# Kernel optimization log

Measured on AMD Instinct MI355X. Metric: run time of the kernel, lower is better.

Reference implementation:

```python
import jax, jax.numpy as jnp
import numpy as np

OBS, ACT, LAT, H = 64, 32, 25, 5
B = 8192
SUP_H = 64


def setup_inputs() -> dict:
    key = jax.random.key(0)
    ks = jax.random.split(key, 12)
    s = 0.1
    inp = {
        'obs': jax.random.normal(ks[0], (B, OBS), jnp.float32),
        # supervisor FeedForward: OBS -> 64 -> 64 -> LAT, ReLU hidden, Sigmoid output
        'sw1': jax.random.normal(ks[1], (OBS, SUP_H), jnp.float32) * s,
        'sb1': jnp.zeros((SUP_H,), jnp.float32),
        'sw2': jax.random.normal(ks[2], (SUP_H, SUP_H), jnp.float32) * s,
        'sb2': jnp.zeros((SUP_H,), jnp.float32),
        'sw3': jax.random.normal(ks[3], (SUP_H, LAT), jnp.float32) * s,
        'sb3': jnp.zeros((LAT,), jnp.float32),
        # OBS*ACT tiny reflex FeedForwards 1 -> H -> 1, stacked into batched params
        'rw1': jax.random.normal(ks[4], (OBS, ACT, H), jnp.float32) * s,
        'rb1': jnp.zeros((OBS, ACT, H), jnp.float32),
        'rw2': jax.random.normal(ks[5], (OBS, ACT, H), jnp.float32) * s,
        'rb2': jnp.zeros((OBS, ACT), jnp.float32),
        # activation matrix (LAT, OBS, ACT)
        'act_matrix': jnp.ones((LAT, OBS, ACT), jnp.float32),
    }
    return inp


def reference(obs, sw1, sb1, sw2, sb2, sw3, sb3, rw1, rb1, rw2, rb2, act_matrix):
    # supervisor: (B, LAT) sigmoid latent activations
    h = jax.nn.relu(obs @ sw1 + sb1)
    h = jax.nn.relu(h @ sw2 + sb2)
    latent = jax.nn.sigmoid(h @ sw3 + sb3)

    # reflex gating: (B, LAT) x (LAT, OBS, ACT) -> (B, OBS, ACT), softmax over ACT
    logits = jnp.einsum('bl,loa->boa', latent, act_matrix)
    reflex_acts = jax.nn.softmax(logits, axis=-1)

    # all OBS*ACT tiny 1->H->1 MLPs, batched: input is obs[:, o] (scalar per net)
    # hidden: (B, OBS, ACT, H)
    rh = jax.nn.relu(obs[:, :, None, None] * rw1[None] + rb1[None])
    reflex_out = jnp.einsum('boah,oah->boa', rh, rw2) + rb2[None]  # (B, OBS, ACT)

    # weighted sum over obs dim -> (B, ACT)
    return jnp.sum(reflex_out * reflex_acts, axis=1)
```

## Files before the change

### kernel.cpp

```cpp
#include <hip/hip_runtime.h>


#define TOBS 64
#define TACT 32
#define TLAT 25
#define TH   5
#define TB   8192
#define BT   16
#define OCH  8
#define NCHUNK (TOBS / OCH)
#define LATP 29
#define OSTR 68

__device__ __forceinline__ float sigmoidf_(float x) {
    return 1.0f / (1.0f + __expf(-x));
}

__global__ __launch_bounds__(256, 2)
void reflex_fused(const float* __restrict__ obs,
                  const float* __restrict__ sw1, const float* __restrict__ sb1,
                  const float* __restrict__ sw2, const float* __restrict__ sb2,
                  const float* __restrict__ sw3, const float* __restrict__ sb3,
                  const float* __restrict__ rw1, const float* __restrict__ rb1,
                  const float* __restrict__ rw2, const float* __restrict__ rb2,
                  const float* __restrict__ am,  float* __restrict__ out)
{
    __shared__ __align__(16) float obs_s[BT * OSTR];
    __shared__ __align__(16) float h1_s[BT * OSTR];
    __shared__ __align__(16) float h2_s[BT * OSTR];
    __shared__ __align__(16) float lat_s[BT * 28];
    __shared__ __align__(16) float sb1_s[64];
    __shared__ __align__(16) float sb2_s[64];
    __shared__ __align__(16) float sb3_s[32];
    __shared__ __align__(16) union {
        struct { float w1[64 * 64]; float w2[64 * 64]; float w3[64 * 26]; } p1;
        struct { float At[OCH * TACT * LATP];
                 float w1[TH * OCH * TACT]; float b1[TH * OCH * TACT];
                 float w2[TH * OCH * TACT]; float b2[OCH * TACT]; } p2;
    } U;

    const int tid  = threadIdx.x;
    const int row0 = blockIdx.x * BT;

    for (int i = tid; i < BT * TOBS; i += 256) {
        int r = i >> 6, k = i & 63;
        obs_s[r * OSTR + k] = obs[(row0 + r) * TOBS + k];
    }
    for (int i = tid; i < 64 * 64; i += 256) U.p1.w1[i] = sw1[i];
    for (int i = tid; i < 64 * 64; i += 256) U.p1.w2[i] = sw2[i];
    for (int i = tid; i < 64 * 25; i += 256) {
        int k = i / 25, j = i - k * 25;
        U.p1.w3[k * 26 + j] = sw3[i];
    }
    if (tid < 64) { sb1_s[tid] = sb1[tid]; sb2_s[tid] = sb2[tid]; }
    if (tid < 32) sb3_s[tid] = (tid < TLAT) ? sb3[tid] : 0.0f;
    __syncthreads();

    {
        const int r = tid >> 4, q = tid & 15, j0 = q * 4;
        float a0 = sb1_s[j0], a1 = sb1_s[j0 + 1], a2 = sb1_s[j0 + 2], a3 = sb1_s[j0 + 3];
        #pragma unroll 8
        for (int k = 0; k < 64; ++k) {
            float x = obs_s[r * OSTR + k];
            const float4 w = *(const float4*)&U.p1.w1[k * 64 + j0];
            a0 = fmaf(x, w.x, a0); a1 = fmaf(x, w.y, a1);
            a2 = fmaf(x, w.z, a2); a3 = fmaf(x, w.w, a3);
        }
        float4 hv = make_float4(fmaxf(a0, 0.f), fmaxf(a1, 0.f), fmaxf(a2, 0.f), fmaxf(a3, 0.f));
        *(float4*)&h1_s[r * OSTR + j0] = hv;
    }
    __syncthreads();

    {
        const int r = tid >> 4, q = tid & 15, j0 = q * 4;
        float a0 = sb2_s[j0], a1 = sb2_s[j0 + 1], a2 = sb2_s[j0 + 2], a3 = sb2_s[j0 + 3];
        #pragma unroll 8
        for (int k = 0; k < 64; ++k) {
            float x = h1_s[r * OSTR + k];
            const float4 w = *(const float4*)&U.p1.w2[k * 64 + j0];
            a0 = fmaf(x, w.x, a0); a1 = fmaf(x, w.y, a1);
            a2 = fmaf(x, w.z, a2); a3 = fmaf(x, w.w, a3);
        }
        float4 hv = make_float4(fmaxf(a0, 0.f), fmaxf(a1, 0.f), fmaxf(a2, 0.f), fmaxf(a3, 0.f));
        *(float4*)&h2_s[r * OSTR + j0] = hv;
    }
    __syncthreads();

    {
        const int r = tid >> 4, q = tid & 15, j = q * 2;
        float a0 = sb3_s[j & 31], a1 = sb3_s[(j + 1) & 31];
        #pragma unroll 8
        for (int k = 0; k < 64; ++k) {
            float x = h2_s[r * OSTR + k];
            a0 = fmaf(x, U.p1.w3[k * 26 + j], a0);
            a1 = fmaf(x, U.p1.w3[k * 26 + j + 1], a1);
        }
        if (j < TLAT)     lat_s[r * 28 + j]     = sigmoidf_(a0);
        if (j + 1 < TLAT) lat_s[r * 28 + j + 1] = sigmoidf_(a1);
    }
    __syncthreads();

    const int lane = tid & 63;
    const int a    = lane & 31;
    const int hw   = tid >> 5;
    const int r0   = hw * 2, r1 = hw * 2 + 1;

    float latA[TLAT], latB[TLAT];
    #pragma unroll
    for (int l = 0; l < TLAT; ++l) {
        latA[l] = lat_s[r0 * 28 + l];
        latB[l] = lat_s[r1 * 28 + l];
    }
    float acc0 = 0.f, acc1 = 0.f;

    for (int c = 0; c < NCHUNK; ++c) {
        const int o0 = c * OCH;
        __syncthreads();

        {
            const int oc = tid >> 5, a_ = tid & 31;
            const int o  = o0 + oc;
            #pragma unroll
            for (int l = 0; l < TLAT; ++l)
                U.p2.At[tid * LATP + l] = am[(l * TOBS + o) * TACT + a_];
        }
        for (int i = tid; i < TH * OCH * TACT; i += 256) {
            int h = i >> 8, j = i & 255;
            int o = o0 + (j >> 5), a_ = j & 31;
            int gi = (o * TACT + a_) * TH + h;
            U.p2.w1[i] = rw1[gi];
            U.p2.b1[i] = rb1[gi];
            U.p2.w2[i] = rw2[gi];
        }
        for (int i = tid; i < OCH * TACT; i += 256)
            U.p2.b2[i] = rb2[(o0 + (i >> 5)) * TACT + (i & 31)];
        __syncthreads();

        for (int oc = 0; oc < OCH; ++oc) {
            const int o  = o0 + oc;
            const int jb = oc * TACT + a;

            float l0 = 0.f, l1 = 0.f;
            const int ab = jb * LATP;
            #pragma unroll
            for (int l = 0; l < TLAT; ++l) {
                float Av = U.p2.At[ab + l];
                l0 = fmaf(Av, latA[l], l0);
                l1 = fmaf(Av, latB[l], l1);
            }
            float e0 = __expf(l0), e1 = __expf(l1);

            float s0 = e0, s1 = e1;
            #pragma unroll
            for (int d = 16; d >= 1; d >>= 1) {
                s0 += __shfl_xor(s0, d);
                s1 += __shfl_xor(s1, d);
            }
            float p0 = e0 * __builtin_amdgcn_rcpf(s0);
            float p1 = e1 * __builtin_amdgcn_rcpf(s1);

            float x0 = obs_s[r0 * OSTR + o], x1 = obs_s[r1 * OSTR + o];
            float ro0 = U.p2.b2[jb], ro1 = ro0;
            #pragma unroll
            for (int h = 0; h < TH; ++h) {
                float w1v = U.p2.w1[h * 256 + jb];
                float b1v = U.p2.b1[h * 256 + jb];
                float w2v = U.p2.w2[h * 256 + jb];
                float t0 = fmaxf(fmaf(x0, w1v, b1v), 0.f);
                float t1 = fmaxf(fmaf(x1, w1v, b1v), 0.f);
                ro0 = fmaf(t0, w2v, ro0);
                ro1 = fmaf(t1, w2v, ro1);
            }
            acc0 = fmaf(ro0, p0, acc0);
            acc1 = fmaf(ro1, p1, acc1);
        }
    }

    out[(row0 + r0) * TACT + a] = acc0;
    out[(row0 + r1) * TACT + a] = acc1;
}

extern "C" void kernel_launch(void* const* d_in, const int* in_sizes, int n_in,
                              void* d_out, int out_size, void* d_ws, size_t ws_size,
                              hipStream_t stream) {
    const float* obs = (const float*)d_in[0];
    const float* sw1 = (const float*)d_in[1];
    const float* sb1 = (const float*)d_in[2];
    const float* sw2 = (const float*)d_in[3];
    const float* sb2 = (const float*)d_in[4];
    const float* sw3 = (const float*)d_in[5];
    const float* sb3 = (const float*)d_in[6];
    const float* rw1 = (const float*)d_in[7];
    const float* rb1 = (const float*)d_in[8];
    const float* rw2 = (const float*)d_in[9];
    const float* rb2 = (const float*)d_in[10];
    const float* am  = (const float*)d_in[11];
    float* out = (float*)d_out;

    reflex_fused<<<TB / BT, 256, 0, stream>>>(obs, sw1, sb1, sw2, sb2, sw3, sb3,
                                              rw1, rb1, rw2, rb2, am, out);
}
```

Measured before the change: 63.64 us.

## Double-buffer reflex parameter chunks with register prefetch and DPP reductions

The reflex-stage chunks (activation matrix slice and per-net weights) are now double-buffered: the next chunk is loaded from global memory into registers while the current chunk is computed, then written to the alternate shared buffer, which halves the barriers per chunk. Supervisor MLP weights are read straight from global memory instead of being staged in shared memory, which shrinks shared usage. Shared layouts are padded so each thread reads its data with float4 loads, and the softmax sum uses DPP/swizzle instead of shuffles. The risks are higher register pressure from the prefetch arrays and more global weight traffic in the MLP stages.

```diff
diff --git a/kernel.cpp b/kernel.cpp
--- a/kernel.cpp
+++ b/kernel.cpp
@@ -7,10 +7,24 @@
 #define TH   5
 #define TB   8192
 #define BT   16
-#define OCH  8
-#define NCHUNK (TOBS / OCH)
-#define LATP 29
-#define OSTR 68
+#define OCH  4
+#define NCH  16
+#define ATS  28
+#define WTS  20
+#define HSTR 68
+
+#define DPP_ADD(x, ctrl) \
+  ((x) + __builtin_bit_cast(float, __builtin_amdgcn_update_dpp( \
+      0, __builtin_bit_cast(int, (x)), (ctrl), 0xF, 0xF, true)))
+
+__device__ __forceinline__ float halfwave_sum(float x) {
+    x = DPP_ADD(x, 0xB1);
+    x = DPP_ADD(x, 0x4E);
+    x = DPP_ADD(x, 0x141);
+    x = DPP_ADD(x, 0x140);
+    int y = __builtin_amdgcn_ds_swizzle(__builtin_bit_cast(int, x), 0x401F);
+    return x + __builtin_bit_cast(float, y);
+}
 
 __device__ __forceinline__ float sigmoidf_(float x) {
     return 1.0f / (1.0f + __expf(-x));
@@ -25,154 +39,187 @@
                   const float* __restrict__ rw2, const float* __restrict__ rb2,
                   const float* __restrict__ am,  float* __restrict__ out)
 {
-    __shared__ __align__(16) float obs_s[BT * OSTR];
-    __shared__ __align__(16) float h1_s[BT * OSTR];
-    __shared__ __align__(16) float h2_s[BT * OSTR];
-    __shared__ __align__(16) float lat_s[BT * 28];
-    __shared__ __align__(16) float sb1_s[64];
-    __shared__ __align__(16) float sb2_s[64];
-    __shared__ __align__(16) float sb3_s[32];
+    __shared__ __align__(16) float obs_s[BT * HSTR];
+    __shared__ __align__(16) float lat_s[BT * 26];
     __shared__ __align__(16) union {
-        struct { float w1[64 * 64]; float w2[64 * 64]; float w3[64 * 26]; } p1;
-        struct { float At[OCH * TACT * LATP];
-                 float w1[TH * OCH * TACT]; float b1[TH * OCH * TACT];
-                 float w2[TH * OCH * TACT]; float b2[OCH * TACT]; } p2;
+        struct { float h1[BT * HSTR]; float h2[BT * HSTR]; } p1;
+        struct { float At[2][128 * ATS]; float Wt[2][128 * WTS]; } p2;
     } U;
 
     const int tid  = threadIdx.x;
     const int row0 = blockIdx.x * BT;
 
-    for (int i = tid; i < BT * TOBS; i += 256) {
-        int r = i >> 6, k = i & 63;
-        obs_s[r * OSTR + k] = obs[(row0 + r) * TOBS + k];
-    }
-    for (int i = tid; i < 64 * 64; i += 256) U.p1.w1[i] = sw1[i];
-    for (int i = tid; i < 64 * 64; i += 256) U.p1.w2[i] = sw2[i];
-    for (int i = tid; i < 64 * 25; i += 256) {
-        int k = i / 25, j = i - k * 25;
-        U.p1.w3[k * 26 + j] = sw3[i];
-    }
-    if (tid < 64) { sb1_s[tid] = sb1[tid]; sb2_s[tid] = sb2[tid]; }
-    if (tid < 32) sb3_s[tid] = (tid < TLAT) ? sb3[tid] : 0.0f;
-    __syncthreads();
-
-    {
-        const int r = tid >> 4, q = tid & 15, j0 = q * 4;
-        float a0 = sb1_s[j0], a1 = sb1_s[j0 + 1], a2 = sb1_s[j0 + 2], a3 = sb1_s[j0 + 3];
+    {
+        const int r = tid >> 4, f = tid & 15;
+        *(float4*)&obs_s[r * HSTR + f * 4] =
+            *(const float4*)&obs[(row0 + r) * TOBS + f * 4];
+    }
+    __syncthreads();
+
+    {
+        const int r = tid >> 4, j0 = (tid & 15) * 4;
+        float4 acc = *(const float4*)&sb1[j0];
         #pragma unroll 8
         for (int k = 0; k < 64; ++k) {
-            float x = obs_s[r * OSTR + k];
-            const float4 w = *(const float4*)&U.p1.w1[k * 64 + j0];
-            a0 = fmaf(x, w.x, a0); a1 = fmaf(x, w.y, a1);
-            a2 = fmaf(x, w.z, a2); a3 = fmaf(x, w.w, a3);
-        }
-        float4 hv = make_float4(fmaxf(a0, 0.f), fmaxf(a1, 0.f), fmaxf(a2, 0.f), fmaxf(a3, 0.f));
-        *(float4*)&h1_s[r * OSTR + j0] = hv;
-    }
-    __syncthreads();
-
-    {
-        const int r = tid >> 4, q = tid & 15, j0 = q * 4;
-        float a0 = sb2_s[j0], a1 = sb2_s[j0 + 1], a2 = sb2_s[j0 + 2], a3 = sb2_s[j0 + 3];
+            float x = obs_s[r * HSTR + k];
+            const float4 w = *(const float4*)&sw1[k * 64 + j0];
+            acc.x = fmaf(x, w.x, acc.x); acc.y = fmaf(x, w.y, acc.y);
+            acc.z = fmaf(x, w.z, acc.z); acc.w = fmaf(x, w.w, acc.w);
+        }
+        *(float4*)&U.p1.h1[r * HSTR + j0] =
+            make_float4(fmaxf(acc.x, 0.f), fmaxf(acc.y, 0.f),
+                        fmaxf(acc.z, 0.f), fmaxf(acc.w, 0.f));
+    }
+    __syncthreads();
+
+    {
+        const int r = tid >> 4, j0 = (tid & 15) * 4;
+        float4 acc = *(const float4*)&sb2[j0];
         #pragma unroll 8
         for (int k = 0; k < 64; ++k) {
-            float x = h1_s[r * OSTR + k];
-            const float4 w = *(const float4*)&U.p1.w2[k * 64 + j0];
-            a0 = fmaf(x, w.x, a0); a1 = fmaf(x, w.y, a1);
-            a2 = fmaf(x, w.z, a2); a3 = fmaf(x, w.w, a3);
-        }
-        float4 hv = make_float4(fmaxf(a0, 0.f), fmaxf(a1, 0.f), fmaxf(a2, 0.f), fmaxf(a3, 0.f));
-        *(float4*)&h2_s[r * OSTR + j0] = hv;
-    }
-    __syncthreads();
-
-    {
-        const int r = tid >> 4, q = tid & 15, j = q * 2;
-        float a0 = sb3_s[j & 31], a1 = sb3_s[(j + 1) & 31];
-        #pragma unroll 8
-        for (int k = 0; k < 64; ++k) {
-            float x = h2_s[r * OSTR + k];
-            a0 = fmaf(x, U.p1.w3[k * 26 + j], a0);
-            a1 = fmaf(x, U.p1.w3[k * 26 + j + 1], a1);
-        }
-        if (j < TLAT)     lat_s[r * 28 + j]     = sigmoidf_(a0);
-        if (j + 1 < TLAT) lat_s[r * 28 + j + 1] = sigmoidf_(a1);
-    }
-    __syncthreads();
-
-    const int lane = tid & 63;
-    const int a    = lane & 31;
-    const int hw   = tid >> 5;
-    const int r0   = hw * 2, r1 = hw * 2 + 1;
-
+            float x = U.p1.h1[r * HSTR + k];
+            const float4 w = *(const float4*)&sw2[k * 64 + j0];
+            acc.x = fmaf(x, w.x, acc.x); acc.y = fmaf(x, w.y, acc.y);
+            acc.z = fmaf(x, w.z, acc.z); acc.w = fmaf(x, w.w, acc.w);
+        }
+        *(float4*)&U.p1.h2[r * HSTR + j0] =
+            make_float4(fmaxf(acc.x, 0.f), fmaxf(acc.y, 0.f),
+                        fmaxf(acc.z, 0.f), fmaxf(acc.w, 0.f));
+    }
+    __syncthreads();
+
+    {
+        const int r = tid >> 4, q = tid & 15;
+        if (q < 13) {
+            const int j = q * 2;
+            float a0 = sb3[j];
+            float a1 = (j + 1 < TLAT) ? sb3[j + 1] : 0.f;
+            #pragma unroll 8
+            for (int k = 0; k < 64; ++k) {
+                float x = U.p1.h2[r * HSTR + k];
+                a0 = fmaf(x, sw3[k * TLAT + j], a0);
+                if (j + 1 < TLAT) a1 = fmaf(x, sw3[k * TLAT + j + 1], a1);
+            }
+            lat_s[r * 26 + j] = sigmoidf_(a0);
+            if (j + 1 < TLAT) lat_s[r * 26 + j + 1] = sigmoidf_(a1);
+        }
+    }
+
+    const int a  = tid & 31;
+    const int hw = tid >> 5;
+    const int r0 = hw * 2, r1 = r0 + 1;
+
+    float pA[13], pW[8], pB2 = 0.f;
+
+    auto stage_load = [&](int c) {
+        const int o0 = c * OCH;
+        const float* amc = am + o0 * TACT;
+        #pragma unroll
+        for (int t = 0; t < 13; ++t) {
+            int i = tid + t * 256;
+            if (i < 3200) {
+                int l = i >> 7, jb = i & 127;
+                pA[t] = amc[l * (TOBS * TACT) + jb];
+            }
+        }
+        const int base160 = o0 * 160;
+        #pragma unroll
+        for (int t = 0; t < 8; ++t) {
+            int i = tid + t * 256;
+            if (i < 1920) {
+                int arr = i / 640, rem = i - arr * 640;
+                const float* p = (arr == 0) ? rw1 : ((arr == 1) ? rb1 : rw2);
+                pW[t] = p[base160 + rem];
+            }
+        }
+        if (tid < 128) pB2 = rb2[o0 * TACT + tid];
+    };
+
+    auto stage_write = [&](int b) {
+        float* Ab = U.p2.At[b];
+        #pragma unroll
+        for (int t = 0; t < 13; ++t) {
+            int i = tid + t * 256;
+            if (i < 3200) {
+                int l = i >> 7, jb = i & 127;
+                Ab[jb * ATS + l] = pA[t];
+            }
+        }
+        float* Wb = U.p2.Wt[b];
+        #pragma unroll
+        for (int t = 0; t < 8; ++t) {
+            int i = tid + t * 256;
+            if (i < 1920) {
+                int arr = i / 640, rem = i - arr * 640;
+                int g = rem / 5, h = rem - g * 5;
+                Wb[g * WTS + arr * 5 + h] = pW[t];
+            }
+        }
+        if (tid < 128) Wb[tid * WTS + 15] = pB2;
+    };
+
+    stage_load(0);
+    __syncthreads();
     float latA[TLAT], latB[TLAT];
     #pragma unroll
     for (int l = 0; l < TLAT; ++l) {
-        latA[l] = lat_s[r0 * 28 + l];
-        latB[l] = lat_s[r1 * 28 + l];
-    }
+        latA[l] = lat_s[r0 * 26 + l];
+        latB[l] = lat_s[r1 * 26 + l];
+    }
+    stage_write(0);
+    __syncthreads();
+
     float acc0 = 0.f, acc1 = 0.f;
 
-    for (int c = 0; c < NCHUNK; ++c) {
-        const int o0 = c * OCH;
-        __syncthreads();
+    for (int c = 0; c < NCH; ++c) {
+        if (c + 1 < NCH) stage_load(c + 1);
 
         {
-            const int oc = tid >> 5, a_ = tid & 31;
-            const int o  = o0 + oc;
+            const float* Ab = U.p2.At[c & 1];
+            const float* Wb = U.p2.Wt[c & 1];
             #pragma unroll
-            for (int l = 0; l < TLAT; ++l)
-                U.p2.At[tid * LATP + l] = am[(l * TOBS + o) * TACT + a_];
-        }
-        for (int i = tid; i < TH * OCH * TACT; i += 256) {
-            int h = i >> 8, j = i & 255;
-            int o = o0 + (j >> 5), a_ = j & 31;
-            int gi = (o * TACT + a_) * TH + h;
-            U.p2.w1[i] = rw1[gi];
-            U.p2.b1[i] = rb1[gi];
-            U.p2.w2[i] = rw2[gi];
-        }
-        for (int i = tid; i < OCH * TACT; i += 256)
-            U.p2.b2[i] = rb2[(o0 + (i >> 5)) * TACT + (i & 31)];
-        __syncthreads();
-
-        for (int oc = 0; oc < OCH; ++oc) {
-            const int o  = o0 + oc;
-            const int jb = oc * TACT + a;
-
-            float l0 = 0.f, l1 = 0.f;
-            const int ab = jb * LATP;
-            #pragma unroll
-            for (int l = 0; l < TLAT; ++l) {
-                float Av = U.p2.At[ab + l];
-                l0 = fmaf(Av, latA[l], l0);
-                l1 = fmaf(Av, latB[l], l1);
-            }
-            float e0 = __expf(l0), e1 = __expf(l1);
-
-            float s0 = e0, s1 = e1;
-            #pragma unroll
-            for (int d = 16; d >= 1; d >>= 1) {
-                s0 += __shfl_xor(s0, d);
-                s1 += __shfl_xor(s1, d);
-            }
-            float p0 = e0 * __builtin_amdgcn_rcpf(s0);
-            float p1 = e1 * __builtin_amdgcn_rcpf(s1);
-
-            float x0 = obs_s[r0 * OSTR + o], x1 = obs_s[r1 * OSTR + o];
-            float ro0 = U.p2.b2[jb], ro1 = ro0;
-            #pragma unroll
-            for (int h = 0; h < TH; ++h) {
-                float w1v = U.p2.w1[h * 256 + jb];
-                float b1v = U.p2.b1[h * 256 + jb];
-                float w2v = U.p2.w2[h * 256 + jb];
-                float t0 = fmaxf(fmaf(x0, w1v, b1v), 0.f);
-                float t1 = fmaxf(fmaf(x1, w1v, b1v), 0.f);
-                ro0 = fmaf(t0, w2v, ro0);
-                ro1 = fmaf(t1, w2v, ro1);
-            }
-            acc0 = fmaf(ro0, p0, acc0);
-            acc1 = fmaf(ro1, p1, acc1);
+            for (int oc = 0; oc < OCH; ++oc) {
+                const int o  = c * OCH + oc;
+                const int jb = oc * TACT + a;
+
+                float Af[28];
+                const float4* A4 = (const float4*)&Ab[jb * ATS];
+                #pragma unroll
+                for (int t = 0; t < 7; ++t) *(float4*)&Af[4 * t] = A4[t];
+
+                float l0 = 0.f, l1 = 0.f;
+                #pragma unroll
+                for (int l = 0; l < TLAT; ++l) {
+                    l0 = fmaf(Af[l], latA[l], l0);
+                    l1 = fmaf(Af[l], latB[l], l1);
+                }
+                float e0 = __expf(l0), e1 = __expf(l1);
+                float s0 = halfwave_sum(e0), s1 = halfwave_sum(e1);
+                float p0 = e0 * __builtin_amdgcn_rcpf(s0);
+                float p1 = e1 * __builtin_amdgcn_rcpf(s1);
+
+                float wv[16];
+                const float4* W4 = (const float4*)&Wb[jb * WTS];
+                #pragma unroll
+                for (int t = 0; t < 4; ++t) *(float4*)&wv[4 * t] = W4[t];
+
+                float x0 = obs_s[r0 * HSTR + o], x1 = obs_s[r1 * HSTR + o];
+                float ro0 = wv[15], ro1 = wv[15];
+                #pragma unroll
+                for (int h = 0; h < TH; ++h) {
+                    float t0 = fmaxf(fmaf(x0, wv[h], wv[5 + h]), 0.f);
+                    float t1 = fmaxf(fmaf(x1, wv[h], wv[5 + h]), 0.f);
+                    ro0 = fmaf(t0, wv[10 + h], ro0);
+                    ro1 = fmaf(t1, wv[10 + h], ro1);
+                }
+                acc0 = fmaf(ro0, p0, acc0);
+                acc1 = fmaf(ro1, p1, acc1);
+            }
+        }
+
+        if (c + 1 < NCH) {
+            stage_write((c + 1) & 1);
+            __syncthreads();
         }
     }
 
```

New measurement: 189.2 us. 2.97x slower.
